# Kernel optimization log

Measured on AMD Instinct MI355X. Metric: run time of the kernel, lower is better.

## Reference

```python
import jax, jax.numpy as jnp
import numpy as np

DIM = 96
HEADS = 8  # num_heads_v
EPS = 1e-12  # torch F.normalize eps


def conv1x1(x, w, b):
    # x: [B,C,H,W], w: [O,C,1,1], b: [O]
    y = jnp.einsum('bchw,oc->bohw', x, w[:, :, 0, 0])
    return y + b[None, :, None, None]


def dwconv3x3(x, w, b):
    # depthwise 3x3, groups == channels; w: [C,1,3,3]
    y = jax.lax.conv_general_dilated(
        x, w, window_strides=(1, 1), padding=((1, 1), (1, 1)),
        dimension_numbers=('NCHW', 'OIHW', 'NCHW'),
        feature_group_count=x.shape[1])
    return y + b[None, :, None, None]


def setup_inputs() -> dict:
    key = jax.random.key(0)
    ks = jax.random.split(key, 7)
    c = DIM
    s = 0.05
    x = jax.random.normal(ks[0], (4, c, 256, 256), jnp.float32)
    qkv_w = jax.random.normal(ks[1], (3 * c, c, 1, 1), jnp.float32) * s
    qkv_b = jax.random.normal(ks[2], (3 * c,), jnp.float32) * s
    dw_w = jax.random.normal(ks[3], (3 * c, 1, 3, 3), jnp.float32) * s
    dw_b = jax.random.normal(ks[4], (3 * c,), jnp.float32) * s
    proj_w = jax.random.normal(ks[5], (c, c, 1, 1), jnp.float32) * s
    proj_b = jax.random.normal(ks[6], (c,), jnp.float32) * s
    temperature = jnp.ones((HEADS, 1, 1), jnp.float32)
    return {"x": x, "qkv_w": qkv_w, "qkv_b": qkv_b, "dw_w": dw_w,
            "dw_b": dw_b, "proj_w": proj_w, "proj_b": proj_b,
            "temperature": temperature}


def reference(x, qkv_w, qkv_b, dw_w, dw_b, proj_w, proj_b, temperature):
    b, c, h, w = x.shape
    head = temperature.shape[0]
    w2 = w // head
    qkv = dwconv3x3(conv1x1(x, qkv_w, qkv_b), dw_w, dw_b)
    q0, k0, v0 = jnp.split(qkv, 3, axis=1)  # each [b,c,h,w]

    def to_heads(t):
        # 'b c h (head w2) -> b head w2 (c h)'
        t = t.reshape(b, c, h, head, w2)
        return jnp.transpose(t, (0, 3, 4, 1, 2)).reshape(b, head, w2, c * h)

    q = to_heads(q0)
    k = to_heads(k0)
    v = to_heads(v0)
    q = q / jnp.maximum(jnp.linalg.norm(q, axis=-1, keepdims=True), EPS)
    k = k / jnp.maximum(jnp.linalg.norm(k, axis=-1, keepdims=True), EPS)
    attn = jnp.einsum('bhid,bhjd->bhij', q, k) * temperature[None]  # [b,head,w2,w2]
    attn = jax.nn.softmax(attn, axis=-1)
    out = jnp.einsum('bhij,bhjd->bhid', attn, v)  # [b,head,w2,c*h]
    # 'b head w2 (c h) -> b c h (head w2)'
    out = out.reshape(b, head, w2, c, h)
    out = jnp.transpose(out, (0, 3, 4, 1, 2)).reshape(b, c, h, w)
    return conv1x1(out, proj_w, proj_b)
```

## Files before the change

### kernel.cpp

```cpp
#include <hip/hip_runtime.h>

#define CC 96
#define C3 288
#define HH 256
#define WW 256
#define HWC 65536
#define NHEADS 8
#define W2 32

typedef __bf16 bf16x8 __attribute__((ext_vector_type(8)));
typedef float f32x4 __attribute__((ext_vector_type(4)));
typedef unsigned short us8v __attribute__((ext_vector_type(8)));

__device__ __forceinline__ float bf2f(unsigned short u) {
  return __uint_as_float(((unsigned)u) << 16);
}
__device__ __forceinline__ unsigned short f2bf(float f) {
  unsigned u = __float_as_uint(f);
  unsigned r = u + 0x7fffu + ((u >> 16) & 1u);
  return (unsigned short)(r >> 16);
}

__global__ __launch_bounds__(256, 2) void k1_qkv_mfma(
    const float* __restrict__ x, const float* __restrict__ qw,
    const float* __restrict__ qb, unsigned short* __restrict__ pre, int b0)
{
  __shared__ __align__(16) unsigned short As2[2][128 * 106];
  const int t = threadIdx.x;
  const int o0 = blockIdx.y * 96;
  const int bz = blockIdx.z;
  const float* xb = x + (size_t)(b0 + bz) * CC * HWC;

  const int wave = t >> 6, lane = t & 63;
  const int wm = wave & 1, wn = wave >> 1;
  const int row = lane & 15, kg = lane >> 4;

  bf16x8 bfr[3][3];
  float bias[3];
#pragma unroll
  for (int nt = 0; nt < 3; ++nt) {
    int ocl = wn * 48 + nt * 16 + row;
    bias[nt] = qb[o0 + ocl];
#pragma unroll
    for (int kk = 0; kk < 3; ++kk) {
      const float* wp = qw + (size_t)(o0 + ocl) * 96 + kk * 32 + kg * 8;
      float4 w0 = *reinterpret_cast<const float4*>(wp);
      float4 w1 = *reinterpret_cast<const float4*>(wp + 4);
      us8v u;
      u[0] = f2bf(w0.x); u[1] = f2bf(w0.y); u[2] = f2bf(w0.z); u[3] = f2bf(w0.w);
      u[4] = f2bf(w1.x); u[5] = f2bf(w1.y); u[6] = f2bf(w1.z); u[7] = f2bf(w1.w);
      bfr[kk][nt] = *reinterpret_cast<bf16x8*>(&u);
    }
  }

  int sic[6], sp4[6];
#pragma unroll
  for (int r = 0; r < 6; ++r) {
    int lin = r * 256 + t;
    sic[r] = lin >> 5;
    sp4[r] = (lin & 31) * 4;
  }

  int p0 = blockIdx.x * 512;
  float4 va0[6], va1[6];
#pragma unroll
  for (int r = 0; r < 6; ++r) {
    va0[r] = *reinterpret_cast<const float4*>(xb + (size_t)(2 * sic[r]) * HWC + p0 + sp4[r]);
    va1[r] = *reinterpret_cast<const float4*>(xb + (size_t)(2 * sic[r] + 1) * HWC + p0 + sp4[r]);
  }

  for (int i = 0; i < 4; ++i) {
    unsigned short* Ac = As2[i & 1];
#pragma unroll
    for (int r = 0; r < 6; ++r) {
      float a0[4] = {va0[r].x, va0[r].y, va0[r].z, va0[r].w};
      float a1[4] = {va1[r].x, va1[r].y, va1[r].z, va1[r].w};
#pragma unroll
      for (int j = 0; j < 4; ++j) {
        unsigned pk = (unsigned)f2bf(a0[j]) | ((unsigned)f2bf(a1[j]) << 16);
        *reinterpret_cast<unsigned*>(&Ac[(sp4[r] + j) * 106 + 2 * sic[r]]) = pk;
      }
    }
    if (i < 3) {
      int p0n = p0 + 128;
#pragma unroll
      for (int r = 0; r < 6; ++r) {
        va0[r] = *reinterpret_cast<const float4*>(xb + (size_t)(2 * sic[r]) * HWC + p0n + sp4[r]);
        va1[r] = *reinterpret_cast<const float4*>(xb + (size_t)(2 * sic[r] + 1) * HWC + p0n + sp4[r]);
      }
    }
    __syncthreads();

    f32x4 acc[4][3];
#pragma unroll
    for (int mt = 0; mt < 4; ++mt)
#pragma unroll
      for (int nt = 0; nt < 3; ++nt) acc[mt][nt] = (f32x4){0.f, 0.f, 0.f, 0.f};
#pragma unroll
    for (int kk = 0; kk < 3; ++kk) {
      bf16x8 a[4];
#pragma unroll
      for (int mt = 0; mt < 4; ++mt)
        a[mt] = *reinterpret_cast<const bf16x8*>(
            &Ac[(wm * 64 + mt * 16 + row) * 106 + kk * 32 + kg * 8]);
#pragma unroll
      for (int mt = 0; mt < 4; ++mt)
#pragma unroll
        for (int nt = 0; nt < 3; ++nt)
          acc[mt][nt] = __builtin_amdgcn_mfma_f32_16x16x32_bf16(
              a[mt], bfr[kk][nt], acc[mt][nt], 0, 0, 0);
    }
    __syncthreads();

    unsigned short* tD = Ac;
#pragma unroll
    for (int nt = 0; nt < 3; ++nt) {
      int ocl = wn * 48 + nt * 16 + row;
      float bv = bias[nt];
#pragma unroll
      for (int mt = 0; mt < 4; ++mt) {
        int pxl = wm * 64 + mt * 16 + kg * 4;
        f32x4 v = acc[mt][nt];
        unsigned pk0 = (unsigned)f2bf(v[0] + bv) | ((unsigned)f2bf(v[1] + bv) << 16);
        unsigned pk1 = (unsigned)f2bf(v[2] + bv) | ((unsigned)f2bf(v[3] + bv) << 16);
        *reinterpret_cast<unsigned*>(&tD[ocl * 136 + pxl]) = pk0;
        *reinterpret_cast<unsigned*>(&tD[ocl * 136 + pxl + 2]) = pk1;
      }
    }
    __syncthreads();
    unsigned short* preb = pre + ((size_t)bz * C3 + o0) * HWC + p0;
#pragma unroll
    for (int r = 0; r < 6; ++r) {
      int lin = r * 256 + t;
      int oc = lin >> 4, ch = lin & 15;
      us8v v = *reinterpret_cast<const us8v*>(&tD[oc * 136 + ch * 8]);
      *reinterpret_cast<us8v*>(preb + (size_t)oc * HWC + ch * 8) = v;
    }
    p0 += 128;
  }
}

__global__ __launch_bounds__(256) void k2_dw(
    const unsigned short* __restrict__ pre, const float* __restrict__ dww,
    const float* __restrict__ dwb, unsigned short* __restrict__ dwo)
{
  const int t = threadIdx.x;
  const int c3 = blockIdx.x;
  const int hb = blockIdx.y;
  const int bz = blockIdx.z;
  const size_t choff = ((size_t)bz * C3 + c3) * HWC;
  const int team = t >> 5, tl = t & 31;
  const int h0 = hb * 32 + team * 4;

  us8v rin[6];
#pragma unroll
  for (int r = 0; r < 6; ++r) {
    int hh = h0 - 1 + r;
    if (hh >= 0 && hh < HH)
      rin[r] = *reinterpret_cast<const us8v*>(pre + choff + (size_t)hh * WW + tl * 8);
    else
      rin[r] = (us8v){0, 0, 0, 0, 0, 0, 0, 0};
  }

  float wg[9];
#pragma unroll
  for (int i = 0; i < 9; ++i) wg[i] = dww[c3 * 9 + i];
  const float bias = dwb[c3];

  float f[6][8];
  float lf[6], rt[6];
#pragma unroll
  for (int r = 0; r < 6; ++r) {
#pragma unroll
    for (int j = 0; j < 8; ++j) f[r][j] = bf2f(rin[r][j]);
    float l = __shfl_up(f[r][7], 1, 32);
    float rr = __shfl_down(f[r][0], 1, 32);
    lf[r] = (tl == 0) ? 0.f : l;
    rt[r] = (tl == 31) ? 0.f : rr;
  }

#pragma unroll
  for (int orow = 0; orow < 4; ++orow) {
    float o[8];
#pragma unroll
    for (int j = 0; j < 8; ++j) o[j] = bias;
#pragma unroll
    for (int k = 0; k < 3; ++k) {
      const int r = orow + k;
      const float w0 = wg[k * 3 + 0], w1 = wg[k * 3 + 1], w2 = wg[k * 3 + 2];
      o[0] = fmaf(lf[r], w0, fmaf(f[r][0], w1, fmaf(f[r][1], w2, o[0])));
#pragma unroll
      for (int j = 1; j < 7; ++j)
        o[j] = fmaf(f[r][j - 1], w0, fmaf(f[r][j], w1, fmaf(f[r][j + 1], w2, o[j])));
      o[7] = fmaf(f[r][6], w0, fmaf(f[r][7], w1, fmaf(rt[r], w2, o[7])));
    }
    us8v u;
#pragma unroll
    for (int j = 0; j < 8; ++j) u[j] = f2bf(o[j]);
    *reinterpret_cast<us8v*>((unsigned short*)dwo + choff + (size_t)(h0 + orow) * WW + tl * 8) = u;
  }
}

__global__ __launch_bounds__(256) void k3_gram(
    const unsigned short* __restrict__ dwo, float* __restrict__ gpart,
    float* __restrict__ ssq)
{
  __shared__ float qs[256 * 32];
  __shared__ float ks[256 * 32];
  const int t = threadIdx.x;
  const int c = blockIdx.x, head = blockIdx.y, bz = blockIdx.z;
  const unsigned short* qp = dwo + ((size_t)bz * C3 + c) * HWC + head * W2;
  const unsigned short* kp = dwo + ((size_t)bz * C3 + CC + c) * HWC + head * W2;
  ushort4 qu[8], ku[8];
#pragma unroll
  for (int it = 0; it < 8; ++it) {
    int lin = it * 256 + t;
    int h = lin >> 3, j4 = (lin & 7) * 4;
    qu[it] = *reinterpret_cast<const ushort4*>(qp + h * WW + j4);
    ku[it] = *reinterpret_cast<const ushort4*>(kp + h * WW + j4);
  }
  __builtin_amdgcn_sched_barrier(0);
#pragma unroll
  for (int it = 0; it < 8; ++it) {
    int lin = it * 256 + t;
    int h = lin >> 3, j4 = (lin & 7) * 4;
    *reinterpret_cast<float4*>(&qs[h * 32 + j4]) =
        make_float4(bf2f(qu[it].x), bf2f(qu[it].y), bf2f(qu[it].z), bf2f(qu[it].w));
    *reinterpret_cast<float4*>(&ks[h * 32 + j4]) =
        make_float4(bf2f(ku[it].x), bf2f(ku[it].y), bf2f(ku[it].z), bf2f(ku[it].w));
  }
  __syncthreads();
  const int i = t & 31, jg = t >> 5;
  float a0 = 0, a1 = 0, a2 = 0, a3 = 0;
  for (int h = 0; h < 256; ++h) {
    float qv = qs[h * 32 + i];
    float4 kv = *reinterpret_cast<const float4*>(&ks[h * 32 + jg * 4]);
    a0 = fmaf(qv, kv.x, a0); a1 = fmaf(qv, kv.y, a1);
    a2 = fmaf(qv, kv.z, a2); a3 = fmaf(qv, kv.w, a3);
  }
  float* gp = gpart + (((size_t)bz * NHEADS + head) * CC + c) * 1024;
  gp[(jg * 4 + 0) * 32 + i] = a0;
  gp[(jg * 4 + 1) * 32 + i] = a1;
  gp[(jg * 4 + 2) * 32 + i] = a2;
  gp[(jg * 4 + 3) * 32 + i] = a3;
  if (t < 64) {
    const float* src = (t < 32) ? qs : ks;
    const int col = t & 31;
    float ssum = 0;
    for (int h = 0; h < 256; ++h) { float v = src[h * 32 + col]; ssum = fmaf(v, v, ssum); }
    atomicAdd(&ssq[((size_t)bz * 2 + (t >> 5)) * 256 + head * W2 + col], ssum);
  }
}

__global__ __launch_bounds__(256) void k4a_reduce(
    const float* __restrict__ gpart, float* __restrict__ g)
{
  __shared__ float l[256];
  const int t = threadIdx.x;
  const int head = blockIdx.x, chunk = blockIdx.y, bz = blockIdx.z;
  const int e = chunk * 128 + (t & 127);
  const int half = t >> 7;
  const float* gp = gpart + (((size_t)bz * NHEADS + head) * CC + half * 48) * 1024 + e;
  float s = 0.f;
#pragma unroll 4
  for (int c = 0; c < 48; ++c) s += gp[(size_t)c * 1024];
  l[t] = s;
  __syncthreads();
  if (t < 128)
    g[((size_t)bz * NHEADS + head) * 1024 + chunk * 128 + t] = l[t] + l[t + 128];
}

__global__ __launch_bounds__(64) void k4b_softmax(
    const float* __restrict__ g, const float* __restrict__ ssq,
    const float* __restrict__ temp, float* __restrict__ attn)
{
  const int t = threadIdx.x;
  const int head = blockIdx.x, bz = blockIdx.y;
  if (t >= 32) return;
  const int i = t;
  const float* gb = g + ((size_t)bz * NHEADS + head) * 1024;
  const float* sq_ = ssq + (size_t)bz * 512 + head * W2;
  const float* sk_ = ssq + (size_t)bz * 512 + 256 + head * W2;
  float invq = 1.f / fmaxf(sqrtf(sq_[i]), 1e-12f);
  float tpq = temp[head] * invq;
  float row[32];
  float m = -1e30f;
#pragma unroll
  for (int j = 0; j < 32; ++j) {
    float invk = 1.f / fmaxf(sqrtf(sk_[j]), 1e-12f);
    float v = gb[j * 32 + i] * tpq * invk;
    row[j] = v;
    m = fmaxf(m, v);
  }
  float ssum = 0;
#pragma unroll
  for (int j = 0; j < 32; ++j) { row[j] = expf(row[j] - m); ssum += row[j]; }
  float inv = 1.f / ssum;
  float* ap = attn + ((size_t)bz * NHEADS + head) * 1024 + i * 32;
#pragma unroll
  for (int j = 0; j < 32; ++j) ap[j] = row[j] * inv;
}

__global__ __launch_bounds__(256) void k5a_attnv(
    const unsigned short* __restrict__ dwo, const float* __restrict__ attn,
    unsigned short* __restrict__ tbuf)
{
  __shared__ __align__(16) unsigned short vsm[64 * 264];
  __shared__ __align__(16) unsigned short atn_s[256 * 36];
  const int t = threadIdx.x;
  const int tile = blockIdx.x;
  const int bz = blockIdx.y;
  const size_t R0 = (size_t)tile * 64;
  const unsigned short* vsrc = dwo + ((size_t)bz * C3 + 2 * CC) * HWC + R0 * 256;

  us8v vv[8];
#pragma unroll
  for (int j = 0; j < 8; ++j)
    vv[j] = *reinterpret_cast<const us8v*>(vsrc + (size_t)(j * 256 + t) * 8);
  float4 av[8];
  {
    const float* ap = attn + (size_t)bz * 8192 + t * 32;
#pragma unroll
    for (int k = 0; k < 8; ++k)
      av[k] = *reinterpret_cast<const float4*>(ap + k * 4);
  }
  __builtin_amdgcn_sched_barrier(0);
#pragma unroll
  for (int j = 0; j < 8; ++j) {
    int n = j * 256 + t;
    int row = n >> 5, c8 = n & 31;
    *reinterpret_cast<us8v*>(&vsm[row * 264 + c8 * 8]) = vv[j];
  }
#pragma unroll
  for (int k = 0; k < 8; ++k) {
    ushort4 u;
    u.x = f2bf(av[k].x); u.y = f2bf(av[k].y); u.z = f2bf(av[k].z); u.w = f2bf(av[k].w);
    *reinterpret_cast<ushort4*>(&atn_s[t * 36 + k * 4]) = u;
  }
  __syncthreads();

  const int wave = t >> 6, lane = t & 63;
  const int mrow = lane & 15, kg = lane >> 4;

  bf16x8 a[8], b[16];
#pragma unroll
  for (int hd = 0; hd < 8; ++hd)
    a[hd] = *reinterpret_cast<const bf16x8*>(
        &vsm[(wave * 16 + mrow) * 264 + hd * 32 + kg * 8]);
#pragma unroll
  for (int hd = 0; hd < 8; ++hd)
#pragma unroll
    for (int it = 0; it < 2; ++it)
      b[hd * 2 + it] = *reinterpret_cast<const bf16x8*>(
          &atn_s[(hd * 32 + it * 16 + mrow) * 36 + kg * 8]);

  f32x4 acc[16];
#pragma unroll
  for (int q = 0; q < 16; ++q) acc[q] = (f32x4){0.f, 0.f, 0.f, 0.f};
#pragma unroll
  for (int hd = 0; hd < 8; ++hd)
#pragma unroll
    for (int it = 0; it < 2; ++it)
      acc[hd * 2 + it] = __builtin_amdgcn_mfma_f32_16x16x32_bf16(
          a[hd], b[hd * 2 + it], acc[hd * 2 + it], 0, 0, 0);
  __syncthreads();

#pragma unroll
  for (int hd = 0; hd < 8; ++hd)
#pragma unroll
    for (int it = 0; it < 2; ++it) {
      f32x4 v = acc[hd * 2 + it];
      int col = hd * 32 + it * 16 + mrow;
#pragma unroll
      for (int r = 0; r < 4; ++r)
        vsm[(wave * 16 + kg * 4 + r) * 264 + col] = f2bf(v[r]);
    }
  unsigned short* tdst = tbuf + (size_t)bz * CC * HWC + R0 * 256;
#pragma unroll
  for (int k = 0; k < 8; ++k) {
    int n = k * 64 + lane;
    int rloc = n >> 5, c8 = n & 31;
    us8v v = *reinterpret_cast<const us8v*>(&vsm[(wave * 16 + rloc) * 264 + c8 * 8]);
    *reinterpret_cast<us8v*>(tdst + ((size_t)(wave * 16 + rloc)) * 256 + c8 * 8) = v;
  }
}

__global__ __launch_bounds__(256) void k5b_proj(
    const unsigned short* __restrict__ tbuf, const float* __restrict__ pw,
    const float* __restrict__ pb, float* __restrict__ out, int b0)
{
  __shared__ __align__(16) char smem[50688];
  unsigned short* As = (unsigned short*)smem;
  unsigned short* Ws = (unsigned short*)(smem + 27136);
  float* tD = (float*)smem;
  const int t = threadIdx.x;
  const int p0 = blockIdx.x * 128;
  const int bz = blockIdx.y;
  const unsigned short* tb = tbuf + (size_t)bz * CC * HWC;

  us8v ua0[3], ua1[3];
#pragma unroll
  for (int r = 0; r < 3; ++r) {
    int lin = r * 256 + t;
    int icp = lin >> 4, p8 = (lin & 15) * 8;
    ua0[r] = *reinterpret_cast<const us8v*>(tb + (size_t)(2 * icp) * HWC + p0 + p8);
    ua1[r] = *reinterpret_cast<const us8v*>(tb + (size_t)(2 * icp + 1) * HWC + p0 + p8);
  }
  float4 vw[9];
#pragma unroll
  for (int r = 0; r < 9; ++r) {
    int lin = r * 256 + t;
    int oc = lin / 24;
    int ic4 = (lin - oc * 24) * 4;
    vw[r] = *reinterpret_cast<const float4*>(pw + (size_t)oc * 96 + ic4);
  }
  __builtin_amdgcn_sched_barrier(0);
#pragma unroll
  for (int r = 0; r < 3; ++r) {
    int lin = r * 256 + t;
    int icp = lin >> 4, p8 = (lin & 15) * 8;
#pragma unroll
    for (int j = 0; j < 8; ++j) {
      unsigned pk = (unsigned)ua0[r][j] | ((unsigned)ua1[r][j] << 16);
      *reinterpret_cast<unsigned*>(&As[(p8 + j) * 106 + 2 * icp]) = pk;
    }
  }
#pragma unroll
  for (int r = 0; r < 9; ++r) {
    int lin = r * 256 + t;
    int oc = lin / 24;
    int ic4 = (lin - oc * 24) * 4;
    ushort4 u;
    u.x = f2bf(vw[r].x); u.y = f2bf(vw[r].y); u.z = f2bf(vw[r].z); u.w = f2bf(vw[r].w);
    *reinterpret_cast<ushort4*>(&Ws[oc * 106 + ic4]) = u;
  }
  __syncthreads();

  const int wave = t >> 6, lane = t & 63;
  const int wm = wave & 1, wn = wave >> 1;
  const int row = lane & 15, kg = lane >> 4;

  f32x4 acc[4][3];
#pragma unroll
  for (int mt = 0; mt < 4; ++mt)
#pragma unroll
    for (int nt = 0; nt < 3; ++nt) acc[mt][nt] = (f32x4){0.f, 0.f, 0.f, 0.f};

#pragma unroll
  for (int kk = 0; kk < 3; ++kk) {
    bf16x8 a[4], b[3];
#pragma unroll
    for (int mt = 0; mt < 4; ++mt)
      a[mt] = *reinterpret_cast<const bf16x8*>(
          &As[(wm * 64 + mt * 16 + row) * 106 + kk * 32 + kg * 8]);
#pragma unroll
    for (int nt = 0; nt < 3; ++nt)
      b[nt] = *reinterpret_cast<const bf16x8*>(
          &Ws[(wn * 48 + nt * 16 + row) * 106 + kk * 32 + kg * 8]);
#pragma unroll
    for (int mt = 0; mt < 4; ++mt)
#pragma unroll
      for (int nt = 0; nt < 3; ++nt)
        acc[mt][nt] = __builtin_amdgcn_mfma_f32_16x16x32_bf16(
            a[mt], b[nt], acc[mt][nt], 0, 0, 0);
  }
  __syncthreads();

#pragma unroll
  for (int nt = 0; nt < 3; ++nt) {
    int ocl = wn * 48 + nt * 16 + row;
    float bv = pb[ocl];
#pragma unroll
    for (int mt = 0; mt < 4; ++mt) {
      int pxl = wm * 64 + mt * 16 + kg * 4;
      f32x4 v = acc[mt][nt];
      float4 w = make_float4(v[0] + bv, v[1] + bv, v[2] + bv, v[3] + bv);
      *reinterpret_cast<float4*>(&tD[ocl * 132 + pxl]) = w;
    }
  }
  __syncthreads();
  float* ob = out + (size_t)(b0 + bz) * CC * HWC + p0;
#pragma unroll
  for (int r = 0; r < 12; ++r) {
    int lin = r * 256 + t;
    int o = lin >> 5, p4 = (lin & 31) * 4;
    float4 v = *reinterpret_cast<const float4*>(&tD[o * 132 + p4]);
    *reinterpret_cast<float4*>(ob + (size_t)o * HWC + p4) = v;
  }
}

extern "C" void kernel_launch(void* const* d_in, const int* in_sizes, int n_in,
                              void* d_out, int out_size, void* d_ws, size_t ws_size,
                              hipStream_t stream)
{
  const float* x      = (const float*)d_in[0];
  const float* qkv_w  = (const float*)d_in[1];
  const float* qkv_b  = (const float*)d_in[2];
  const float* dw_w   = (const float*)d_in[3];
  const float* dw_b   = (const float*)d_in[4];
  const float* proj_w = (const float*)d_in[5];
  const float* proj_b = (const float*)d_in[6];
  const float* temp   = (const float*)d_in[7];
  float* out = (float*)d_out;

  const size_t per_pre  = (size_t)C3 * HWC * 2;
  const size_t per_gp   = (size_t)NHEADS * CC * 1024 * 4;
  const size_t per_ssq  = (size_t)2 * 256 * 4;
  const size_t per_attn = (size_t)NHEADS * 1024 * 4;
  const size_t per_g    = (size_t)NHEADS * 1024 * 4;
  const size_t per_b = per_pre * 2 + per_gp + per_ssq + per_attn + per_g;

  int bc = 4;
  while (bc > 1 && per_b * (size_t)bc > ws_size) bc >>= 1;

  char* p = (char*)d_ws;
  unsigned short* pre = (unsigned short*)p; p += per_pre * bc;
  unsigned short* dwo = (unsigned short*)p; p += per_pre * bc;
  float* gpart = (float*)p; p += per_gp * bc;
  float* ssq   = (float*)p; p += per_ssq * bc;
  float* attn  = (float*)p; p += per_attn * bc;
  float* g     = (float*)p; p += per_g * bc;
  unsigned short* tbuf = pre;

  for (int b0 = 0; b0 < 4; b0 += bc) {
    k1_qkv_mfma<<<dim3(128, 3, bc), 256, 0, stream>>>(x, qkv_w, qkv_b, pre, b0);
    k2_dw<<<dim3(C3, 8, bc), 256, 0, stream>>>(pre, dw_w, dw_b, dwo);
    hipMemsetAsync(ssq, 0, per_ssq * bc, stream);
    k3_gram<<<dim3(CC, NHEADS, bc), 256, 0, stream>>>(dwo, gpart, ssq);
    k4a_reduce<<<dim3(NHEADS, 8, bc), 256, 0, stream>>>(gpart, g);
    k4b_softmax<<<dim3(NHEADS, bc), 64, 0, stream>>>(g, ssq, temp, attn);
    k5a_attnv<<<dim3(384, bc), 256, 0, stream>>>(dwo, attn, tbuf);
    k5b_proj<<<dim3(512, bc), 256, 0, stream>>>(tbuf, proj_w, proj_b, out, b0);
  }
}
```

Before: 269.8 us.

## Shrink LDS tiles for higher occupancy; pipeline gram and proj kernels

The QKV GEMM kernel halves its pixel tile to 64, which cuts LDS use and lets it ask for 4 blocks per CU, at the cost of more loop iterations and an added barrier. The gram kernel now stages Q/K in two 128-row halves, prefetching the second half while computing on the first, and spreads the sum-of-squares work over all threads instead of 64. The projection kernel is rebuilt like k1: weights held in registers, a double-buffered 64-pixel loop, and 4x fewer blocks. The aim is better latency hiding through occupancy and overlap, with the risk of extra synchronisation and less parallelism per launch.

Result: slower. 279.8 us (+3.7%).

```diff
diff --git a/kernel.cpp b/kernel.cpp
--- a/kernel.cpp
+++ b/kernel.cpp
@@ -21,11 +21,11 @@
   return (unsigned short)(r >> 16);
 }
 
-__global__ __launch_bounds__(256, 2) void k1_qkv_mfma(
+__global__ __launch_bounds__(256, 4) void k1_qkv_mfma(
     const float* __restrict__ x, const float* __restrict__ qw,
     const float* __restrict__ qb, unsigned short* __restrict__ pre, int b0)
 {
-  __shared__ __align__(16) unsigned short As2[2][128 * 106];
+  __shared__ __align__(16) unsigned short As2[2][64 * 106];
   const int t = threadIdx.x;
   const int o0 = blockIdx.y * 96;
   const int bz = blockIdx.z;
@@ -53,26 +53,26 @@
     }
   }
 
-  int sic[6], sp4[6];
-#pragma unroll
-  for (int r = 0; r < 6; ++r) {
+  int sic[3], sp4[3];
+#pragma unroll
+  for (int r = 0; r < 3; ++r) {
     int lin = r * 256 + t;
-    sic[r] = lin >> 5;
-    sp4[r] = (lin & 31) * 4;
+    sic[r] = lin >> 4;
+    sp4[r] = (lin & 15) * 4;
   }
 
   int p0 = blockIdx.x * 512;
-  float4 va0[6], va1[6];
-#pragma unroll
-  for (int r = 0; r < 6; ++r) {
+  float4 va0[3], va1[3];
+#pragma unroll
+  for (int r = 0; r < 3; ++r) {
     va0[r] = *reinterpret_cast<const float4*>(xb + (size_t)(2 * sic[r]) * HWC + p0 + sp4[r]);
     va1[r] = *reinterpret_cast<const float4*>(xb + (size_t)(2 * sic[r] + 1) * HWC + p0 + sp4[r]);
   }
 
-  for (int i = 0; i < 4; ++i) {
+  for (int i = 0; i < 8; ++i) {
     unsigned short* Ac = As2[i & 1];
 #pragma unroll
-    for (int r = 0; r < 6; ++r) {
+    for (int r = 0; r < 3; ++r) {
       float a0[4] = {va0[r].x, va0[r].y, va0[r].z, va0[r].w};
       float a1[4] = {va1[r].x, va1[r].y, va1[r].z, va1[r].w};
 #pragma unroll
@@ -81,30 +81,30 @@
         *reinterpret_cast<unsigned*>(&Ac[(sp4[r] + j) * 106 + 2 * sic[r]]) = pk;
       }
     }
-    if (i < 3) {
-      int p0n = p0 + 128;
-#pragma unroll
-      for (int r = 0; r < 6; ++r) {
+    if (i < 7) {
+      int p0n = p0 + 64;
+#pragma unroll
+      for (int r = 0; r < 3; ++r) {
         va0[r] = *reinterpret_cast<const float4*>(xb + (size_t)(2 * sic[r]) * HWC + p0n + sp4[r]);
         va1[r] = *reinterpret_cast<const float4*>(xb + (size_t)(2 * sic[r] + 1) * HWC + p0n + sp4[r]);
       }
     }
     __syncthreads();
 
-    f32x4 acc[4][3];
-#pragma unroll
-    for (int mt = 0; mt < 4; ++mt)
+    f32x4 acc[2][3];
+#pragma unroll
+    for (int mt = 0; mt < 2; ++mt)
 #pragma unroll
       for (int nt = 0; nt < 3; ++nt) acc[mt][nt] = (f32x4){0.f, 0.f, 0.f, 0.f};
 #pragma unroll
     for (int kk = 0; kk < 3; ++kk) {
-      bf16x8 a[4];
-#pragma unroll
-      for (int mt = 0; mt < 4; ++mt)
+      bf16x8 a[2];
+#pragma unroll
+      for (int mt = 0; mt < 2; ++mt)
         a[mt] = *reinterpret_cast<const bf16x8*>(
-            &Ac[(wm * 64 + mt * 16 + row) * 106 + kk * 32 + kg * 8]);
-#pragma unroll
-      for (int mt = 0; mt < 4; ++mt)
+            &Ac[(wm * 32 + mt * 16 + row) * 106 + kk * 32 + kg * 8]);
+#pragma unroll
+      for (int mt = 0; mt < 2; ++mt)
 #pragma unroll
         for (int nt = 0; nt < 3; ++nt)
           acc[mt][nt] = __builtin_amdgcn_mfma_f32_16x16x32_bf16(
@@ -112,31 +112,32 @@
     }
     __syncthreads();
 
-    unsigned short* tD = Ac;
+    unsigned short* tD = (unsigned short*)As2;
 #pragma unroll
     for (int nt = 0; nt < 3; ++nt) {
       int ocl = wn * 48 + nt * 16 + row;
       float bv = bias[nt];
 #pragma unroll
-      for (int mt = 0; mt < 4; ++mt) {
-        int pxl = wm * 64 + mt * 16 + kg * 4;
+      for (int mt = 0; mt < 2; ++mt) {
+        int pxl = wm * 32 + mt * 16 + kg * 4;
         f32x4 v = acc[mt][nt];
         unsigned pk0 = (unsigned)f2bf(v[0] + bv) | ((unsigned)f2bf(v[1] + bv) << 16);
         unsigned pk1 = (unsigned)f2bf(v[2] + bv) | ((unsigned)f2bf(v[3] + bv) << 16);
-        *reinterpret_cast<unsigned*>(&tD[ocl * 136 + pxl]) = pk0;
-        *reinterpret_cast<unsigned*>(&tD[ocl * 136 + pxl + 2]) = pk1;
+        *reinterpret_cast<unsigned*>(&tD[ocl * 72 + pxl]) = pk0;
+        *reinterpret_cast<unsigned*>(&tD[ocl * 72 + pxl + 2]) = pk1;
       }
     }
     __syncthreads();
     unsigned short* preb = pre + ((size_t)bz * C3 + o0) * HWC + p0;
 #pragma unroll
-    for (int r = 0; r < 6; ++r) {
+    for (int r = 0; r < 3; ++r) {
       int lin = r * 256 + t;
-      int oc = lin >> 4, ch = lin & 15;
-      us8v v = *reinterpret_cast<const us8v*>(&tD[oc * 136 + ch * 8]);
+      int oc = lin >> 3, ch = lin & 7;
+      us8v v = *reinterpret_cast<const us8v*>(&tD[oc * 72 + ch * 8]);
       *reinterpret_cast<us8v*>(preb + (size_t)oc * HWC + ch * 8) = v;
     }
-    p0 += 128;
+    __syncthreads();
+    p0 += 64;
   }
 }
 
@@ -205,51 +206,70 @@
     const unsigned short* __restrict__ dwo, float* __restrict__ gpart,
     float* __restrict__ ssq)
 {
-  __shared__ float qs[256 * 32];
-  __shared__ float ks[256 * 32];
+  __shared__ float qs[128 * 32];
+  __shared__ float ks[128 * 32];
   const int t = threadIdx.x;
   const int c = blockIdx.x, head = blockIdx.y, bz = blockIdx.z;
   const unsigned short* qp = dwo + ((size_t)bz * C3 + c) * HWC + head * W2;
   const unsigned short* kp = dwo + ((size_t)bz * C3 + CC + c) * HWC + head * W2;
-  ushort4 qu[8], ku[8];
-#pragma unroll
-  for (int it = 0; it < 8; ++it) {
+
+  const int i = t & 31, jg = t >> 5;
+  const int scol = t & 31, stens = t >> 7, shq = (t >> 5) & 3;
+  float a0 = 0, a1 = 0, a2 = 0, a3 = 0, ss = 0;
+
+  ushort4 qu[4], ku[4];
+#pragma unroll
+  for (int it = 0; it < 4; ++it) {
     int lin = it * 256 + t;
     int h = lin >> 3, j4 = (lin & 7) * 4;
     qu[it] = *reinterpret_cast<const ushort4*>(qp + h * WW + j4);
     ku[it] = *reinterpret_cast<const ushort4*>(kp + h * WW + j4);
   }
-  __builtin_amdgcn_sched_barrier(0);
-#pragma unroll
-  for (int it = 0; it < 8; ++it) {
-    int lin = it * 256 + t;
-    int h = lin >> 3, j4 = (lin & 7) * 4;
-    *reinterpret_cast<float4*>(&qs[h * 32 + j4]) =
-        make_float4(bf2f(qu[it].x), bf2f(qu[it].y), bf2f(qu[it].z), bf2f(qu[it].w));
-    *reinterpret_cast<float4*>(&ks[h * 32 + j4]) =
-        make_float4(bf2f(ku[it].x), bf2f(ku[it].y), bf2f(ku[it].z), bf2f(ku[it].w));
-  }
-  __syncthreads();
-  const int i = t & 31, jg = t >> 5;
-  float a0 = 0, a1 = 0, a2 = 0, a3 = 0;
-  for (int h = 0; h < 256; ++h) {
-    float qv = qs[h * 32 + i];
-    float4 kv = *reinterpret_cast<const float4*>(&ks[h * 32 + jg * 4]);
-    a0 = fmaf(qv, kv.x, a0); a1 = fmaf(qv, kv.y, a1);
-    a2 = fmaf(qv, kv.z, a2); a3 = fmaf(qv, kv.w, a3);
-  }
+
+#pragma unroll
+  for (int chn = 0; chn < 2; ++chn) {
+#pragma unroll
+    for (int it = 0; it < 4; ++it) {
+      int lin = it * 256 + t;
+      int h = lin >> 3, j4 = (lin & 7) * 4;
+      *reinterpret_cast<float4*>(&qs[h * 32 + j4]) =
+          make_float4(bf2f(qu[it].x), bf2f(qu[it].y), bf2f(qu[it].z), bf2f(qu[it].w));
+      *reinterpret_cast<float4*>(&ks[h * 32 + j4]) =
+          make_float4(bf2f(ku[it].x), bf2f(ku[it].y), bf2f(ku[it].z), bf2f(ku[it].w));
+    }
+    if (chn == 0) {
+#pragma unroll
+      for (int it = 0; it < 4; ++it) {
+        int lin = it * 256 + t;
+        int h = 128 + (lin >> 3), j4 = (lin & 7) * 4;
+        qu[it] = *reinterpret_cast<const ushort4*>(qp + h * WW + j4);
+        ku[it] = *reinterpret_cast<const ushort4*>(kp + h * WW + j4);
+      }
+    }
+    __syncthreads();
+    for (int h = 0; h < 128; ++h) {
+      float qv = qs[h * 32 + i];
+      float4 kv = *reinterpret_cast<const float4*>(&ks[h * 32 + jg * 4]);
+      a0 = fmaf(qv, kv.x, a0); a1 = fmaf(qv, kv.y, a1);
+      a2 = fmaf(qv, kv.z, a2); a3 = fmaf(qv, kv.w, a3);
+    }
+    {
+      const float* src = stens ? ks : qs;
+#pragma unroll 8
+      for (int k = 0; k < 32; ++k) {
+        float v = src[(shq * 32 + k) * 32 + scol];
+        ss = fmaf(v, v, ss);
+      }
+    }
+    if (chn == 0) __syncthreads();
+  }
+
   float* gp = gpart + (((size_t)bz * NHEADS + head) * CC + c) * 1024;
   gp[(jg * 4 + 0) * 32 + i] = a0;
   gp[(jg * 4 + 1) * 32 + i] = a1;
   gp[(jg * 4 + 2) * 32 + i] = a2;
   gp[(jg * 4 + 3) * 32 + i] = a3;
-  if (t < 64) {
-    const float* src = (t < 32) ? qs : ks;
-    const int col = t & 31;
-    float ssum = 0;
-    for (int h = 0; h < 256; ++h) { float v = src[h * 32 + col]; ssum = fmaf(v, v, ssum); }
-    atomicAdd(&ssq[((size_t)bz * 2 + (t >> 5)) * 256 + head * W2 + col], ssum);
-  }
+  atomicAdd(&ssq[(size_t)bz * 512 + stens * 256 + head * W2 + scol], ss);
 }
 
 __global__ __launch_bounds__(256) void k4a_reduce(
@@ -385,107 +405,120 @@
   }
 }
 
-__global__ __launch_bounds__(256) void k5b_proj(
+__global__ __launch_bounds__(256, 4) void k5b_proj(
     const unsigned short* __restrict__ tbuf, const float* __restrict__ pw,
     const float* __restrict__ pb, float* __restrict__ out, int b0)
 {
-  __shared__ __align__(16) char smem[50688];
-  unsigned short* As = (unsigned short*)smem;
-  unsigned short* Ws = (unsigned short*)(smem + 27136);
-  float* tD = (float*)smem;
-  const int t = threadIdx.x;
-  const int p0 = blockIdx.x * 128;
+  __shared__ __align__(16) unsigned short As2[2][64 * 106];
+  const int t = threadIdx.x;
   const int bz = blockIdx.y;
   const unsigned short* tb = tbuf + (size_t)bz * CC * HWC;
-
-  us8v ua0[3], ua1[3];
-#pragma unroll
-  for (int r = 0; r < 3; ++r) {
-    int lin = r * 256 + t;
-    int icp = lin >> 4, p8 = (lin & 15) * 8;
-    ua0[r] = *reinterpret_cast<const us8v*>(tb + (size_t)(2 * icp) * HWC + p0 + p8);
-    ua1[r] = *reinterpret_cast<const us8v*>(tb + (size_t)(2 * icp + 1) * HWC + p0 + p8);
-  }
-  float4 vw[9];
-#pragma unroll
-  for (int r = 0; r < 9; ++r) {
-    int lin = r * 256 + t;
-    int oc = lin / 24;
-    int ic4 = (lin - oc * 24) * 4;
-    vw[r] = *reinterpret_cast<const float4*>(pw + (size_t)oc * 96 + ic4);
-  }
-  __builtin_amdgcn_sched_barrier(0);
-#pragma unroll
-  for (int r = 0; r < 3; ++r) {
-    int lin = r * 256 + t;
-    int icp = lin >> 4, p8 = (lin & 15) * 8;
-#pragma unroll
-    for (int j = 0; j < 8; ++j) {
-      unsigned pk = (unsigned)ua0[r][j] | ((unsigned)ua1[r][j] << 16);
-      *reinterpret_cast<unsigned*>(&As[(p8 + j) * 106 + 2 * icp]) = pk;
-    }
-  }
-#pragma unroll
-  for (int r = 0; r < 9; ++r) {
-    int lin = r * 256 + t;
-    int oc = lin / 24;
-    int ic4 = (lin - oc * 24) * 4;
-    ushort4 u;
-    u.x = f2bf(vw[r].x); u.y = f2bf(vw[r].y); u.z = f2bf(vw[r].z); u.w = f2bf(vw[r].w);
-    *reinterpret_cast<ushort4*>(&Ws[oc * 106 + ic4]) = u;
-  }
-  __syncthreads();
 
   const int wave = t >> 6, lane = t & 63;
   const int wm = wave & 1, wn = wave >> 1;
   const int row = lane & 15, kg = lane >> 4;
 
-  f32x4 acc[4][3];
-#pragma unroll
-  for (int mt = 0; mt < 4; ++mt)
-#pragma unroll
-    for (int nt = 0; nt < 3; ++nt) acc[mt][nt] = (f32x4){0.f, 0.f, 0.f, 0.f};
-
-#pragma unroll
-  for (int kk = 0; kk < 3; ++kk) {
-    bf16x8 a[4], b[3];
-#pragma unroll
-    for (int mt = 0; mt < 4; ++mt)
-      a[mt] = *reinterpret_cast<const bf16x8*>(
-          &As[(wm * 64 + mt * 16 + row) * 106 + kk * 32 + kg * 8]);
-#pragma unroll
-    for (int nt = 0; nt < 3; ++nt)
-      b[nt] = *reinterpret_cast<const bf16x8*>(
-          &Ws[(wn * 48 + nt * 16 + row) * 106 + kk * 32 + kg * 8]);
-#pragma unroll
-    for (int mt = 0; mt < 4; ++mt)
-#pragma unroll
-      for (int nt = 0; nt < 3; ++nt)
-        acc[mt][nt] = __builtin_amdgcn_mfma_f32_16x16x32_bf16(
-            a[mt], b[nt], acc[mt][nt], 0, 0, 0);
-  }
-  __syncthreads();
-
+  bf16x8 bfr[3][3];
+  float bias[3];
 #pragma unroll
   for (int nt = 0; nt < 3; ++nt) {
     int ocl = wn * 48 + nt * 16 + row;
-    float bv = pb[ocl];
-#pragma unroll
-    for (int mt = 0; mt < 4; ++mt) {
-      int pxl = wm * 64 + mt * 16 + kg * 4;
-      f32x4 v = acc[mt][nt];
-      float4 w = make_float4(v[0] + bv, v[1] + bv, v[2] + bv, v[3] + bv);
-      *reinterpret_cast<float4*>(&tD[ocl * 132 + pxl]) = w;
-    }
-  }
-  __syncthreads();
-  float* ob = out + (size_t)(b0 + bz) * CC * HWC + p0;
-#pragma unroll
-  for (int r = 0; r < 12; ++r) {
+    bias[nt] = pb[ocl];
+#pragma unroll
+    for (int kk = 0; kk < 3; ++kk) {
+      const float* wp = pw + (size_t)ocl * 96 + kk * 32 + kg * 8;
+      float4 w0 = *reinterpret_cast<const float4*>(wp);
+      float4 w1 = *reinterpret_cast<const float4*>(wp + 4);
+      us8v u;
+      u[0] = f2bf(w0.x); u[1] = f2bf(w0.y); u[2] = f2bf(w0.z); u[3] = f2bf(w0.w);
+      u[4] = f2bf(w1.x); u[5] = f2bf(w1.y); u[6] = f2bf(w1.z); u[7] = f2bf(w1.w);
+      bfr[kk][nt] = *reinterpret_cast<bf16x8*>(&u);
+    }
+  }
+
+  int sic[3], sp4[3];
+#pragma unroll
+  for (int r = 0; r < 3; ++r) {
     int lin = r * 256 + t;
-    int o = lin >> 5, p4 = (lin & 31) * 4;
-    float4 v = *reinterpret_cast<const float4*>(&tD[o * 132 + p4]);
-    *reinterpret_cast<float4*>(ob + (size_t)o * HWC + p4) = v;
+    sic[r] = lin >> 4;
+    sp4[r] = (lin & 15) * 4;
+  }
+
+  int p0 = blockIdx.x * 512;
+  ushort4 ua0[3], ua1[3];
+#pragma unroll
+  for (int r = 0; r < 3; ++r) {
+    ua0[r] = *reinterpret_cast<const ushort4*>(tb + (size_t)(2 * sic[r]) * HWC + p0 + sp4[r]);
+    ua1[r] = *reinterpret_cast<const ushort4*>(tb + (size_t)(2 * sic[r] + 1) * HWC + p0 + sp4[r]);
+  }
+
+  for (int i = 0; i < 8; ++i) {
+    unsigned short* Ac = As2[i & 1];
+#pragma unroll
+    for (int r = 0; r < 3; ++r) {
+      unsigned short a0[4] = {ua0[r].x, ua0[r].y, ua0[r].z, ua0[r].w};
+      unsigned short a1[4] = {ua1[r].x, ua1[r].y, ua1[r].z, ua1[r].w};
+#pragma unroll
+      for (int j = 0; j < 4; ++j) {
+        unsigned pk = (unsigned)a0[j] | ((unsigned)a1[j] << 16);
+        *reinterpret_cast<unsigned*>(&Ac[(sp4[r] + j) * 106 + 2 * sic[r]]) = pk;
+      }
+    }
+    if (i < 7) {
+      int p0n = p0 + 64;
+#pragma unroll
+      for (int r = 0; r < 3; ++r) {
+        ua0[r] = *reinterpret_cast<const ushort4*>(tb + (size_t)(2 * sic[r]) * HWC + p0n + sp4[r]);
+        ua1[r] = *reinterpret_cast<const ushort4*>(tb + (size_t)(2 * sic[r] + 1) * HWC + p0n + sp4[r]);
+      }
+    }
+    __syncthreads();
+
+    f32x4 acc[2][3];
+#pragma unroll
+    for (int mt = 0; mt < 2; ++mt)
+#pragma unroll
+      for (int nt = 0; nt < 3; ++nt) acc[mt][nt] = (f32x4){0.f, 0.f, 0.f, 0.f};
+#pragma unroll
+    for (int kk = 0; kk < 3; ++kk) {
+      bf16x8 a[2];
+#pragma unroll
+      for (int mt = 0; mt < 2; ++mt)
+        a[mt] = *reinterpret_cast<const bf16x8*>(
+            &Ac[(wm * 32 + mt * 16 + row) * 106 + kk * 32 + kg * 8]);
+#pragma unroll
+      for (int mt = 0; mt < 2; ++mt)
+#pragma unroll
+        for (int nt = 0; nt < 3; ++nt)
+          acc[mt][nt] = __builtin_amdgcn_mfma_f32_16x16x32_bf16(
+              a[mt], bfr[kk][nt], acc[mt][nt], 0, 0, 0);
+    }
+    __syncthreads();
+
+    float* tD = (float*)As2;
+#pragma unroll
+    for (int nt = 0; nt < 3; ++nt) {
+      int ocl = wn * 48 + nt * 16 + row;
+      float bv = bias[nt];
+#pragma unroll
+      for (int mt = 0; mt < 2; ++mt) {
+        int pxl = wm * 32 + mt * 16 + kg * 4;
+        f32x4 v = acc[mt][nt];
+        float4 w = make_float4(v[0] + bv, v[1] + bv, v[2] + bv, v[3] + bv);
+        *reinterpret_cast<float4*>(&tD[ocl * 68 + pxl]) = w;
+      }
+    }
+    __syncthreads();
+    float* ob = out + (size_t)(b0 + bz) * CC * HWC + p0;
+#pragma unroll
+    for (int r = 0; r < 6; ++r) {
+      int lin = r * 256 + t;
+      int o = lin >> 4, p4 = (lin & 15) * 4;
+      float4 v = *reinterpret_cast<const float4*>(&tD[o * 68 + p4]);
+      *reinterpret_cast<float4*>(ob + (size_t)o * HWC + p4) = v;
+    }
+    __syncthreads();
+    p0 += 64;
   }
 }
 
@@ -530,6 +563,6 @@
     k4a_reduce<<<dim3(NHEADS, 8, bc), 256, 0, stream>>>(gpart, g);
     k4b_softmax<<<dim3(NHEADS, bc), 64, 0, stream>>>(g, ssq, temp, attn);
     k5a_attnv<<<dim3(384, bc), 256, 0, stream>>>(dwo, attn, tbuf);
-    k5b_proj<<<dim3(512, bc), 256, 0, stream>>>(tbuf, proj_w, proj_b, out, b0);
-  }
-}
+    k5b_proj<<<dim3(128, bc), 256, 0, stream>>>(tbuf, proj_w, proj_b, out, b0);
+  }
+}
```
